# Kernel optimization log

Measured on AMD Instinct MI355X. Metric: run time of the kernel, lower is better.

Reference implementation:

```python
import jax, jax.numpy as jnp
import numpy as np

B, D = 8192, 256      # batch, input_dim == n_nodes
ENC = 256             # encoder_dim
DEC = 64              # decoder_dim
THR = 0.1             # adjacency threshold


def setup_inputs() -> dict:
    key = jax.random.key(0)
    ks = jax.random.split(key, 9)
    s = lambda k, sh, fan: jax.random.normal(k, sh, jnp.float32) / np.sqrt(fan).astype(np.float32)
    return {
        "x": jax.random.normal(ks[0], (B, D), jnp.float32),
        "eps": jax.random.normal(ks[1], (B, D), jnp.float32),
        "W_enc": s(ks[2], (D, ENC), D), "b_enc": jnp.zeros((ENC,), jnp.float32),
        "W_mu": s(ks[3], (ENC, D), ENC), "b_mu": jnp.zeros((D,), jnp.float32),
        "W_lv": s(ks[4], (ENC, D), ENC), "b_lv": jnp.zeros((D,), jnp.float32),
        "graph_param": jax.random.normal(ks[5], (D, D), jnp.float32),
        "W_emb": s(ks[6], (D, DEC), 1), "b_emb": jnp.zeros((D, DEC), jnp.float32),
        "W_g1": s(ks[7], (DEC, DEC // 2), DEC), "b_g1": jnp.zeros((DEC // 2,), jnp.float32),
        "W_g2": s(ks[8], (DEC // 2, 1), DEC // 2), "b_g2": jnp.zeros((1,), jnp.float32),
        "iter_": 100,
    }


def _learned_graph(graph_param, iter_):
    # LearnedGraph.forward: sigmoid, force self-loops=1, threshold after iter 50
    g = jax.nn.sigmoid(graph_param)
    eye = jnp.eye(g.shape[0], dtype=g.dtype)
    g = g * (1.0 - eye) + eye
    if iter_ > 50:  # iter_ is a static Python int
        g = jnp.where(g > THR, g, 0.0)  # nn.Threshold(THR, 0)
    return g


def _gcn_norm(adj):
    # DGL GraphConv(norm='both') with edge_weight: messages weighted by adj values,
    # but degree normalization uses structural (unweighted) edge counts.
    mask = (adj != 0).astype(adj.dtype)
    dout = jnp.maximum(mask.sum(1), 1.0)  # out-degree of src j (row sums)
    din = jnp.maximum(mask.sum(0), 1.0)   # in-degree of dst i (col sums)
    # out[i] = sum_j adj[j,i] * x[j] / sqrt(dout[j] * din[i])  ->  M[dst, src]
    return (adj / jnp.sqrt(dout)[:, None] / jnp.sqrt(din)[None, :]).T


def reference(x, eps, W_enc, b_enc, W_mu, b_mu, W_lv, b_lv,
              graph_param, W_emb, b_emb, W_g1, b_g1, W_g2, b_g2, iter_):
    # VAE encoder (Linear + ReLU, then mu/logvar heads)
    h = jax.nn.relu(x @ W_enc + b_enc)
    mu = h @ W_mu + b_mu
    logvar = h @ W_lv + b_lv
    z = mu + eps * jnp.exp(0.5 * logvar)                 # [B, D]
    # learned adjacency over the D feature-nodes
    adj = _learned_graph(graph_param, iter_)             # [D, D]
    # per-feature node embedding: Linear(1, DEC) + tanh per feature
    b_z = jnp.tanh(z[:, :, None] * W_emb[None] + b_emb[None])  # [B, D, DEC]
    # two GraphConv layers (shared adjacency per batch element)
    M = _gcn_norm(adj)                                   # [D, D]
    h1 = jax.nn.relu(jnp.einsum('ij,bjd->bid', M, b_z) @ W_g1 + b_g1)  # [B, D, 32]
    h2 = jnp.einsum('ij,bjd->bid', M, h1) @ W_g2 + b_g2                # [B, D, 1]
    x_hat = h2.reshape(B, -1)                            # [B, D]
    return x_hat, adj, mu, logvar
```

## Files before the change

kernel.cpp:

```cpp
#include <hip/hip_runtime.h>

typedef __bf16 bf16_t;
typedef __bf16 bf16x4 __attribute__((ext_vector_type(4)));
typedef __bf16 bf16x8 __attribute__((ext_vector_type(8)));
typedef float  floatx4 __attribute__((ext_vector_type(4)));

#define MFMA16(a, b, c) __builtin_amdgcn_mfma_f32_16x16x32_bf16((a), (b), (c), 0, 0, 0)

#define ADJ_OFF  2097152
#define MU_OFF   2162688
#define LV_OFF   4259840

#define TWO_LOG2E 2.8853900817779268f

__device__ __forceinline__ float fast_tanh2(float argE2) {
    float e = __builtin_amdgcn_exp2f(argE2);
    return 1.0f - 2.0f * __builtin_amdgcn_rcpf(e + 1.0f);
}

__device__ __forceinline__ bf16x8 cvt8(const float* p) {
    const floatx4 a = *(const floatx4*)p;
    const floatx4 b = *(const floatx4*)(p + 4);
    bf16x8 r;
#pragma unroll
    for (int j = 0; j < 4; j++) { r[j] = (bf16_t)a[j]; r[4 + j] = (bf16_t)b[j]; }
    return r;
}

__global__ __launch_bounds__(256) void k_prep(
    const float* __restrict__ We, const float* __restrict__ Wm,
    const float* __restrict__ Wl, const float* __restrict__ Wemb,
    const float* __restrict__ bemb, bf16_t* __restrict__ Wt,
    bf16_t* __restrict__ wepack, bf16_t* __restrict__ bepack,
    int* __restrict__ colc) {
    __shared__ float tile[64][65];
    const int b = blockIdx.x, tid = threadIdx.x;
    if (b < 48) {
        const int m = b >> 4, t6 = b & 15;
        const int K0 = (t6 >> 2) << 6, N0 = (t6 & 3) << 6;
        const float* src = (m == 0) ? We : ((m == 1) ? Wm : Wl);
#pragma unroll
        for (int p = 0; p < 16; p++) {
            const int idx = p * 256 + tid;
            tile[idx >> 6][idx & 63] = src[(K0 + (idx >> 6)) * 256 + N0 + (idx & 63)];
        }
        __syncthreads();
        bf16_t* dst = Wt + m * 65536;
#pragma unroll
        for (int p = 0; p < 16; p++) {
            const int idx = p * 256 + tid;
            const int nn = idx >> 6, kk = idx & 63;
            dst[(N0 + nn) * 256 + K0 + kk] = (bf16_t)tile[kk][nn];
        }
    } else if (b == 48) {
#pragma unroll 4
        for (int p = 0; p < 64; p++)
            wepack[p * 256 + tid] = (bf16_t)(TWO_LOG2E * Wemb[p * 256 + tid]);
    } else {
        colc[tid] = 0;
#pragma unroll 4
        for (int p = 0; p < 64; p++)
            bepack[p * 256 + tid] = (bf16_t)(TWO_LOG2E * bemb[p * 256 + tid]);
    }
}

__global__ __launch_bounds__(256) void k_deg(
    const float* __restrict__ gp, const int* __restrict__ iterp,
    int* __restrict__ colc, float* __restrict__ rsO) {
    __shared__ unsigned long long mk[4];
    const int j = blockIdx.x, t = threadIdx.x;
    const bool thr = (*iterp) > 50;
    float g = 1.0f / (1.0f + expf(-gp[j * 256 + t]));
    if (t == j) g = 1.0f;
    if (thr && !(g > 0.1f)) g = 0.0f;
    const bool nz = (g != 0.0f);
    const unsigned long long bal = __ballot(nz);
    if ((t & 63) == 0) mk[t >> 6] = bal;
    if (nz) atomicAdd(&colc[t], 1);
    __syncthreads();
    if (t == 0) {
        const int rc = (int)(__popcll(mk[0]) + __popcll(mk[1]) +
                             __popcll(mk[2]) + __popcll(mk[3]));
        rsO[j] = rsqrtf((float)(rc < 1 ? 1 : rc));
    }
}

__global__ __launch_bounds__(256) void k_mkM(
    const float* __restrict__ gp, const int* __restrict__ iterp,
    const int* __restrict__ colc, const float* __restrict__ rsO,
    bf16_t* __restrict__ Mb) {
    const int j = blockIdx.x, t = threadIdx.x;
    const int ci = colc[t];
    const float rsi = rsqrtf((float)(ci < 1 ? 1 : ci));
    float g = 1.0f / (1.0f + expf(-gp[j * 256 + t]));
    if (t == j) g = 1.0f;
    if ((*iterp) > 50 && !(g > 0.1f)) g = 0.0f;
    Mb[t * 256 + j] = (bf16_t)(g * rsO[j] * rsi);
}

__global__ __launch_bounds__(512) void k_ench(
    const float* __restrict__ X, const bf16_t* __restrict__ Wt,
    const float* __restrict__ benc, const float* __restrict__ bmu,
    const float* __restrict__ blv,
    float* __restrict__ MuOut, float* __restrict__ LvOut) {
    __shared__ __align__(16) bf16_t Xs[32 * 264];
    __shared__ __align__(16) bf16_t Hs[32 * 264];
    const bf16_t* Bte = Wt;
    const bf16_t* Btm = Wt + 65536;
    const bf16_t* Btl = Wt + 131072;
    const int tid = threadIdx.x;
    const int r0 = blockIdx.x * 32;
    const int w = tid >> 6;
    const int lane = tid & 63;
    const int n = lane & 15, q = lane >> 4;
    const int cw = w * 32;
    const floatx4 z4 = {0.f, 0.f, 0.f, 0.f};

#pragma unroll
    for (int p = 0; p < 2; p++) {
        const int e0 = (p * 512 + tid) * 8;
        const int row = e0 >> 8, col = e0 & 255;
        *(bf16x8*)(Xs + row * 264 + col) = cvt8(X + (r0 + row) * 256 + col);
    }
    __syncthreads();

    floatx4 ah[2][2];
#pragma unroll
    for (int rt = 0; rt < 2; rt++)
#pragma unroll
        for (int tc = 0; tc < 2; tc++) ah[rt][tc] = z4;
#pragma unroll 2
    for (int k0 = 0; k0 < 256; k0 += 32) {
        bf16x8 a[2], b[2];
#pragma unroll
        for (int rt = 0; rt < 2; rt++)
            a[rt] = *(const bf16x8*)(Xs + (rt * 16 + n) * 264 + k0 + q * 8);
#pragma unroll
        for (int tc = 0; tc < 2; tc++)
            b[tc] = *(const bf16x8*)(Bte + (cw + tc * 16 + n) * 256 + k0 + q * 8);
#pragma unroll
        for (int rt = 0; rt < 2; rt++)
#pragma unroll
            for (int tc = 0; tc < 2; tc++)
                ah[rt][tc] = MFMA16(a[rt], b[tc], ah[rt][tc]);
    }
#pragma unroll
    for (int tc = 0; tc < 2; tc++) {
        const int col = cw + tc * 16 + n;
        const float bv = benc[col];
#pragma unroll
        for (int rt = 0; rt < 2; rt++)
#pragma unroll
            for (int r = 0; r < 4; r++)
                Hs[(rt * 16 + q * 4 + r) * 264 + col] =
                    (bf16_t)fmaxf(ah[rt][tc][r] + bv, 0.0f);
    }
    __syncthreads();

    floatx4 am[2][2], al[2][2];
#pragma unroll
    for (int rt = 0; rt < 2; rt++)
#pragma unroll
        for (int tc = 0; tc < 2; tc++) { am[rt][tc] = z4; al[rt][tc] = z4; }
#pragma unroll 2
    for (int k0 = 0; k0 < 256; k0 += 32) {
        bf16x8 a[2], bm_[2], bl_[2];
#pragma unroll
        for (int rt = 0; rt < 2; rt++)
            a[rt] = *(const bf16x8*)(Hs + (rt * 16 + n) * 264 + k0 + q * 8);
#pragma unroll
        for (int tc = 0; tc < 2; tc++) {
            bm_[tc] = *(const bf16x8*)(Btm + (cw + tc * 16 + n) * 256 + k0 + q * 8);
            bl_[tc] = *(const bf16x8*)(Btl + (cw + tc * 16 + n) * 256 + k0 + q * 8);
        }
#pragma unroll
        for (int rt = 0; rt < 2; rt++)
#pragma unroll
            for (int tc = 0; tc < 2; tc++) {
                am[rt][tc] = MFMA16(a[rt], bm_[tc], am[rt][tc]);
                al[rt][tc] = MFMA16(a[rt], bl_[tc], al[rt][tc]);
            }
    }
#pragma unroll
    for (int tc = 0; tc < 2; tc++) {
        const int col = cw + tc * 16 + n;
        const float bmv = bmu[col], blvv = blv[col];
#pragma unroll
        for (int rt = 0; rt < 2; rt++)
#pragma unroll
            for (int r = 0; r < 4; r++) {
                const int row = r0 + rt * 16 + q * 4 + r;
                MuOut[row * 256 + col] = am[rt][tc][r] + bmv;
                LvOut[row * 256 + col] = al[rt][tc][r] + blvv;
            }
    }
}

__global__ __launch_bounds__(512, 4) void k_gcn(
    const float* __restrict__ Mu, const float* __restrict__ Lv,
    const float* __restrict__ Eps, const bf16_t* __restrict__ wepack,
    const bf16_t* __restrict__ bepack, const float* __restrict__ Wg1,
    const float* __restrict__ bg1, const float* __restrict__ Wg2,
    const bf16_t* __restrict__ Mb, float* __restrict__ Vout) {
    __shared__ __align__(16) bf16_t smem[128 * 256];
    __shared__ float zs[1024];
    const int tid = threadIdx.x;
    const int lane = tid & 63;
    const int w = tid >> 6;
    const int n = lane & 15, q = lane >> 4;
    const int bg = blockIdx.x;
    const floatx4 z4 = {0.f, 0.f, 0.f, 0.f};

    {
        const int gi = bg * 1024 + tid;
        zs[tid] = fmaf(Eps[gi], __expf(0.5f * Lv[gi]), Mu[gi]);
        const int gi2 = gi + 512;
        zs[tid + 512] = fmaf(Eps[gi2], __expf(0.5f * Lv[gi2]), Mu[gi2]);
    }

    bf16x8 wg1f[2][2];
#pragma unroll
    for (int ks = 0; ks < 2; ks++)
#pragma unroll
        for (int te = 0; te < 2; te++)
#pragma unroll
            for (int j = 0; j < 8; j++)
                wg1f[ks][te][j] = (bf16_t)Wg1[(ks * 32 + q * 8 + j) * 32 + te * 16 + n];
    __syncthreads();

#pragma unroll
    for (int jt2 = 0; jt2 < 2; jt2++) {
        const int j0 = (w * 2 + jt2) * 16;
        const int jA = j0 + n;
        const bf16x8 we0 = *(const bf16x8*)(wepack + jA * 64 + q * 8);
        const bf16x8 we1 = *(const bf16x8*)(wepack + jA * 64 + 32 + q * 8);
        const bf16x8 be0 = *(const bf16x8*)(bepack + jA * 64 + q * 8);
        const bf16x8 be1 = *(const bf16x8*)(bepack + jA * 64 + 32 + q * 8);
        const int j8a = (j0 >> 3) + (q >> 1);
        const int jlo = (q & 1) * 4;
        const int sw = ((j8a ^ (n & 7)) << 3) + jlo;
#pragma unroll
        for (int bl = 0; bl < 4; bl++) {
            const float zv = zs[bl * 256 + jA];
            bf16x8 a0, a1;
#pragma unroll
            for (int j = 0; j < 8; j++) {
                a0[j] = (bf16_t)fast_tanh2(fmaf(zv, (float)we0[j], (float)be0[j]));
                a1[j] = (bf16_t)fast_tanh2(fmaf(zv, (float)we1[j], (float)be1[j]));
            }
            floatx4 c0 = z4, c1 = z4;
            c0 = MFMA16(a0, wg1f[0][0], c0);
            c0 = MFMA16(a1, wg1f[1][0], c0);
            c1 = MFMA16(a0, wg1f[0][1], c1);
            c1 = MFMA16(a1, wg1f[1][1], c1);
            bf16x4 s0, s1;
#pragma unroll
            for (int r = 0; r < 4; r++) { s0[r] = (bf16_t)c0[r]; s1[r] = (bf16_t)c1[r]; }
            *(bf16x4*)(smem + (bl * 32 + n) * 256 + sw) = s0;
            *(bf16x4*)(smem + (bl * 32 + 16 + n) * 256 + sw) = s1;
        }
    }
    __syncthreads();

    const int i0 = w * 32;
    floatx4 acc[2][8];
#pragma unroll
    for (int ti = 0; ti < 2; ti++)
#pragma unroll
        for (int tc = 0; tc < 8; tc++) acc[ti][tc] = z4;
#pragma unroll
    for (int k0 = 0; k0 < 256; k0 += 32) {
        const int k8 = k0 >> 3;
        bf16x8 a[2], b[8];
#pragma unroll
        for (int ti = 0; ti < 2; ti++)
            a[ti] = *(const bf16x8*)(Mb + (i0 + ti * 16 + n) * 256 + k0 + q * 8);
#pragma unroll
        for (int tc = 0; tc < 8; tc++)
            b[tc] = *(const bf16x8*)(smem + (tc * 16 + n) * 256 +
                                     (((k8 + q) ^ (n & 7)) << 3));
        __builtin_amdgcn_s_setprio(1);
#pragma unroll
        for (int ti = 0; ti < 2; ti++)
#pragma unroll
            for (int tc = 0; tc < 8; tc++)
                acc[ti][tc] = MFMA16(a[ti], b[tc], acc[ti][tc]);
        __builtin_amdgcn_s_setprio(0);
    }

    const float w2a = Wg2[n],      w2b = Wg2[16 + n];
    const float b1a = bg1[n],      b1b = bg1[16 + n];
    float v32[32];
#pragma unroll
    for (int bl = 0; bl < 4; bl++)
#pragma unroll
        for (int ti = 0; ti < 2; ti++)
#pragma unroll
            for (int r = 0; r < 4; r++)
                v32[bl * 8 + ti * 4 + r] =
                    fmaxf(acc[ti][2 * bl][r] + b1a, 0.0f) * w2a +
                    fmaxf(acc[ti][2 * bl + 1][r] + b1b, 0.0f) * w2b;
    const bool h0 = (lane & 1), h1_ = (lane & 2), h2 = (lane & 4), h3 = (lane & 8);
    float u16[16];
#pragma unroll
    for (int p = 0; p < 16; p++) {
        const float keep = h0 ? v32[2 * p + 1] : v32[2 * p];
        const float send = h0 ? v32[2 * p] : v32[2 * p + 1];
        u16[p] = keep + __shfl_xor(send, 1, 64);
    }
    float u8[8];
#pragma unroll
    for (int p = 0; p < 8; p++) {
        const float keep = h1_ ? u16[2 * p + 1] : u16[2 * p];
        const float send = h1_ ? u16[2 * p] : u16[2 * p + 1];
        u8[p] = keep + __shfl_xor(send, 2, 64);
    }
    float u4[4];
#pragma unroll
    for (int p = 0; p < 4; p++) {
        const float keep = h2 ? u8[2 * p + 1] : u8[2 * p];
        const float send = h2 ? u8[2 * p] : u8[2 * p + 1];
        u4[p] = keep + __shfl_xor(send, 4, 64);
    }
    float u2[2];
#pragma unroll
    for (int p = 0; p < 2; p++) {
        const float keep = h3 ? u4[2 * p + 1] : u4[2 * p];
        const float send = h3 ? u4[2 * p] : u4[2 * p + 1];
        u2[p] = keep + __shfl_xor(send, 8, 64);
    }
    {
        const int i_out = i0 + ((n >> 2) & 1) * 16 + q * 4 + (n & 3);
        const int blv = n >> 3;
        Vout[bg * 1024 + blv * 256 + i_out] = u2[0];
        Vout[bg * 1024 + (2 + blv) * 256 + i_out] = u2[1];
    }
}

__global__ __launch_bounds__(512) void k_out(
    float* __restrict__ VX, const bf16_t* __restrict__ Mb,
    const float* __restrict__ bg2) {
    __shared__ __align__(16) bf16_t va[32 * 264];
    const int tid = threadIdx.x;
    const int lane = tid & 63;
    const int w = tid >> 6;
    const int n = lane & 15, q = lane >> 4;
    const int r0 = blockIdx.x * 32;

#pragma unroll
    for (int p = 0; p < 4; p++) {
        const int i4 = p * 512 + tid;
        const int row = i4 >> 6, c4 = (i4 & 63) * 4;
        const floatx4 v = *(const floatx4*)(VX + (r0 + row) * 256 + c4);
        bf16x4 s;
#pragma unroll
        for (int r = 0; r < 4; r++) s[r] = (bf16_t)v[r];
        *(bf16x4*)(va + row * 264 + c4) = s;
    }
    __syncthreads();

    const int cw = w * 32;
    const floatx4 z4 = {0.f, 0.f, 0.f, 0.f};
    floatx4 acc[2][2];
#pragma unroll
    for (int rt = 0; rt < 2; rt++)
#pragma unroll
        for (int tc = 0; tc < 2; tc++) acc[rt][tc] = z4;
#pragma unroll 2
    for (int k0 = 0; k0 < 256; k0 += 32) {
        bf16x8 a[2], b[2];
#pragma unroll
        for (int rt = 0; rt < 2; rt++)
            a[rt] = *(const bf16x8*)(va + (rt * 16 + n) * 264 + k0 + q * 8);
#pragma unroll
        for (int tc = 0; tc < 2; tc++)
            b[tc] = *(const bf16x8*)(Mb + (cw + tc * 16 + n) * 256 + k0 + q * 8);
#pragma unroll
        for (int rt = 0; rt < 2; rt++)
#pragma unroll
            for (int tc = 0; tc < 2; tc++)
                acc[rt][tc] = MFMA16(a[rt], b[tc], acc[rt][tc]);
    }
    const float bv = bg2[0];
#pragma unroll
    for (int tc = 0; tc < 2; tc++) {
        const int col = cw + tc * 16 + n;
#pragma unroll
        for (int rt = 0; rt < 2; rt++)
#pragma unroll
            for (int r = 0; r < 4; r++)
                VX[(r0 + rt * 16 + q * 4 + r) * 256 + col] = acc[rt][tc][r] + bv;
    }
}

__global__ __launch_bounds__(256) void k_adj(
    const float* __restrict__ gp, const int* __restrict__ iterp,
    float* __restrict__ adjOut) {
    const int o = blockIdx.x * 256 + threadIdx.x;
    const int j = o >> 8, i = o & 255;
    float g = 1.0f / (1.0f + expf(-gp[o]));
    if (i == j) g = 1.0f;
    if ((*iterp) > 50 && !(g > 0.1f)) g = 0.0f;
    adjOut[o] = g;
}

extern "C" void kernel_launch(void* const* d_in, const int* in_sizes, int n_in,
                              void* d_out, int out_size, void* d_ws, size_t ws_size,
                              hipStream_t stream) {
    const float* x    = (const float*)d_in[0];
    const float* eps  = (const float*)d_in[1];
    const float* Wenc = (const float*)d_in[2];
    const float* benc = (const float*)d_in[3];
    const float* Wmu  = (const float*)d_in[4];
    const float* bmu  = (const float*)d_in[5];
    const float* Wlv  = (const float*)d_in[6];
    const float* blv  = (const float*)d_in[7];
    const float* gp   = (const float*)d_in[8];
    const float* Wemb = (const float*)d_in[9];
    const float* bemb = (const float*)d_in[10];
    const float* Wg1  = (const float*)d_in[11];
    const float* bg1  = (const float*)d_in[12];
    const float* Wg2  = (const float*)d_in[13];
    const float* bg2  = (const float*)d_in[14];
    const int*   itr  = (const int*)d_in[15];
    (void)d_ws; (void)ws_size; (void)in_sizes; (void)n_in; (void)out_size;

    float* xhat = (float*)d_out;
    float* adjO = xhat + ADJ_OFF;
    float* muo  = xhat + MU_OFF;
    float* lvo  = xhat + LV_OFF;

    char* adjB = (char*)adjO;
    bf16_t* Mb     = (bf16_t*)adjB;
    bf16_t* wepack = (bf16_t*)(adjB + 131072);
    bf16_t* bepack = (bf16_t*)(adjB + 163840);
    int*    colc   = (int*)(adjB + 196608);
    float*  rsO    = (float*)(adjB + 197632);
    bf16_t* Wt     = (bf16_t*)((char*)d_out + 4194304);

    k_prep<<<dim3(50), dim3(256), 0, stream>>>(Wenc, Wmu, Wlv, Wemb, bemb,
                                               Wt, wepack, bepack, colc);
    k_deg <<<dim3(256), dim3(256), 0, stream>>>(gp, itr, colc, rsO);
    k_mkM <<<dim3(256), dim3(256), 0, stream>>>(gp, itr, colc, rsO, Mb);
    k_ench<<<dim3(256), dim3(512), 0, stream>>>(x, Wt, benc, bmu, blv, muo, lvo);
    k_gcn <<<dim3(2048), dim3(512), 0, stream>>>(muo, lvo, eps, wepack, bepack,
                                                 Wg1, bg1, Wg2, Mb, xhat);
    k_out <<<dim3(256), dim3(512), 0, stream>>>(xhat, Mb, bg2);
    k_adj <<<dim3(256), dim3(256), 0, stream>>>(gp, itr, adjO);
}
```

Before: 198.2 us.

## Split weight prep over more blocks, fuse adj output into mkM via workspace

The weight transpose and pack kernel now uses 32x32 tiles across 208 blocks instead of 50, so more CUs share the prep work. When a workspace buffer is available, scratch data moves there and the adjacency output is written inside k_mkM, which removes the separate k_adj launch. The tanh embedding hoists its bf16-to-float conversions of the weights and biases out of the inner batch loop. The speedup depends on the harness actually providing a large enough workspace; otherwise the old path with k_adj still runs.

```diff
diff --git a/kernel.cpp b/kernel.cpp
--- a/kernel.cpp
+++ b/kernel.cpp
@@ -33,34 +33,40 @@
     const float* __restrict__ bemb, bf16_t* __restrict__ Wt,
     bf16_t* __restrict__ wepack, bf16_t* __restrict__ bepack,
     int* __restrict__ colc) {
-    __shared__ float tile[64][65];
+    __shared__ float tile[32][33];
     const int b = blockIdx.x, tid = threadIdx.x;
-    if (b < 48) {
-        const int m = b >> 4, t6 = b & 15;
-        const int K0 = (t6 >> 2) << 6, N0 = (t6 & 3) << 6;
+    if (b < 192) {
+        const int m = b >> 6, t6 = b & 63;
+        const int K0 = (t6 >> 3) << 5, N0 = (t6 & 7) << 5;
         const float* src = (m == 0) ? We : ((m == 1) ? Wm : Wl);
 #pragma unroll
-        for (int p = 0; p < 16; p++) {
+        for (int p = 0; p < 4; p++) {
             const int idx = p * 256 + tid;
-            tile[idx >> 6][idx & 63] = src[(K0 + (idx >> 6)) * 256 + N0 + (idx & 63)];
+            tile[idx >> 5][idx & 31] = src[(K0 + (idx >> 5)) * 256 + N0 + (idx & 31)];
         }
         __syncthreads();
         bf16_t* dst = Wt + m * 65536;
 #pragma unroll
-        for (int p = 0; p < 16; p++) {
+        for (int p = 0; p < 4; p++) {
             const int idx = p * 256 + tid;
-            const int nn = idx >> 6, kk = idx & 63;
+            const int nn = idx >> 5, kk = idx & 31;
             dst[(N0 + nn) * 256 + K0 + kk] = (bf16_t)tile[kk][nn];
         }
-    } else if (b == 48) {
-#pragma unroll 4
-        for (int p = 0; p < 64; p++)
-            wepack[p * 256 + tid] = (bf16_t)(TWO_LOG2E * Wemb[p * 256 + tid]);
+    } else if (b < 200) {
+        const int base = (b - 192) * 2048;
+#pragma unroll
+        for (int p = 0; p < 8; p++) {
+            const int idx = base + p * 256 + tid;
+            wepack[idx] = (bf16_t)(TWO_LOG2E * Wemb[idx]);
+        }
     } else {
-        colc[tid] = 0;
-#pragma unroll 4
-        for (int p = 0; p < 64; p++)
-            bepack[p * 256 + tid] = (bf16_t)(TWO_LOG2E * bemb[p * 256 + tid]);
+        if (b == 200) colc[tid] = 0;
+        const int base = (b - 200) * 2048;
+#pragma unroll
+        for (int p = 0; p < 8; p++) {
+            const int idx = base + p * 256 + tid;
+            bepack[idx] = (bf16_t)(TWO_LOG2E * bemb[idx]);
+        }
     }
 }
 
@@ -88,13 +94,14 @@
 __global__ __launch_bounds__(256) void k_mkM(
     const float* __restrict__ gp, const int* __restrict__ iterp,
     const int* __restrict__ colc, const float* __restrict__ rsO,
-    bf16_t* __restrict__ Mb) {
+    bf16_t* __restrict__ Mb, float* __restrict__ adjOut) {
     const int j = blockIdx.x, t = threadIdx.x;
     const int ci = colc[t];
     const float rsi = rsqrtf((float)(ci < 1 ? 1 : ci));
     float g = 1.0f / (1.0f + expf(-gp[j * 256 + t]));
     if (t == j) g = 1.0f;
     if ((*iterp) > 50 && !(g > 0.1f)) g = 0.0f;
+    if (adjOut) adjOut[j * 256 + t] = g;
     Mb[t * 256 + j] = (bf16_t)(g * rsO[j] * rsi);
 }
 
@@ -236,6 +243,12 @@
         const bf16x8 we1 = *(const bf16x8*)(wepack + jA * 64 + 32 + q * 8);
         const bf16x8 be0 = *(const bf16x8*)(bepack + jA * 64 + q * 8);
         const bf16x8 be1 = *(const bf16x8*)(bepack + jA * 64 + 32 + q * 8);
+        float wf0[8], wf1[8], bf0[8], bf1[8];
+#pragma unroll
+        for (int j = 0; j < 8; j++) {
+            wf0[j] = (float)we0[j]; wf1[j] = (float)we1[j];
+            bf0[j] = (float)be0[j]; bf1[j] = (float)be1[j];
+        }
         const int j8a = (j0 >> 3) + (q >> 1);
         const int jlo = (q & 1) * 4;
         const int sw = ((j8a ^ (n & 7)) << 3) + jlo;
@@ -245,8 +258,8 @@
             bf16x8 a0, a1;
 #pragma unroll
             for (int j = 0; j < 8; j++) {
-                a0[j] = (bf16_t)fast_tanh2(fmaf(zv, (float)we0[j], (float)be0[j]));
-                a1[j] = (bf16_t)fast_tanh2(fmaf(zv, (float)we1[j], (float)be1[j]));
+                a0[j] = (bf16_t)fast_tanh2(fmaf(zv, wf0[j], bf0[j]));
+                a1[j] = (bf16_t)fast_tanh2(fmaf(zv, wf1[j], bf1[j]));
             }
             floatx4 c0 = z4, c1 = z4;
             c0 = MFMA16(a0, wg1f[0][0], c0);
@@ -423,28 +436,31 @@
     const float* Wg2  = (const float*)d_in[13];
     const float* bg2  = (const float*)d_in[14];
     const int*   itr  = (const int*)d_in[15];
-    (void)d_ws; (void)ws_size; (void)in_sizes; (void)n_in; (void)out_size;
+    (void)in_sizes; (void)n_in; (void)out_size;
 
     float* xhat = (float*)d_out;
     float* adjO = xhat + ADJ_OFF;
     float* muo  = xhat + MU_OFF;
     float* lvo  = xhat + LV_OFF;
 
-    char* adjB = (char*)adjO;
-    bf16_t* Mb     = (bf16_t*)adjB;
-    bf16_t* wepack = (bf16_t*)(adjB + 131072);
-    bf16_t* bepack = (bf16_t*)(adjB + 163840);
-    int*    colc   = (int*)(adjB + 196608);
-    float*  rsO    = (float*)(adjB + 197632);
+    const bool usews = (d_ws != nullptr && ws_size >= 262144);
+    char* scr = usews ? (char*)d_ws : (char*)adjO;
+    bf16_t* Mb     = (bf16_t*)scr;
+    bf16_t* wepack = (bf16_t*)(scr + 131072);
+    bf16_t* bepack = (bf16_t*)(scr + 163840);
+    int*    colc   = (int*)(scr + 196608);
+    float*  rsO    = (float*)(scr + 197632);
     bf16_t* Wt     = (bf16_t*)((char*)d_out + 4194304);
 
-    k_prep<<<dim3(50), dim3(256), 0, stream>>>(Wenc, Wmu, Wlv, Wemb, bemb,
-                                               Wt, wepack, bepack, colc);
+    k_prep<<<dim3(208), dim3(256), 0, stream>>>(Wenc, Wmu, Wlv, Wemb, bemb,
+                                                Wt, wepack, bepack, colc);
     k_deg <<<dim3(256), dim3(256), 0, stream>>>(gp, itr, colc, rsO);
-    k_mkM <<<dim3(256), dim3(256), 0, stream>>>(gp, itr, colc, rsO, Mb);
+    k_mkM <<<dim3(256), dim3(256), 0, stream>>>(gp, itr, colc, rsO, Mb,
+                                                usews ? adjO : nullptr);
     k_ench<<<dim3(256), dim3(512), 0, stream>>>(x, Wt, benc, bmu, blv, muo, lvo);
     k_gcn <<<dim3(2048), dim3(512), 0, stream>>>(muo, lvo, eps, wepack, bepack,
                                                  Wg1, bg1, Wg2, Mb, xhat);
     k_out <<<dim3(256), dim3(512), 0, stream>>>(xhat, Mb, bg2);
-    k_adj <<<dim3(256), dim3(256), 0, stream>>>(gp, itr, adjO);
-}
+    if (!usews)
+        k_adj<<<dim3(256), dim3(256), 0, stream>>>(gp, itr, adjO);
+}
```

New measurement: 192.5 us. 2.9% less time.
